# Optimization experiments

Hardware: AMD Instinct MI355X
Metric: run time of the kernel (lower is better)

Reference implementation:

```python
import jax, jax.numpy as jnp
import numpy as np

B, NV, NDIRS, NRINGS, NCH, NF = 2, 15000, 16, 3, 32, 64


def setup_inputs() -> dict:
    key = jax.random.key(0)
    k1, k2, k3, k4 = jax.random.split(key, 4)
    y = jax.random.normal(k1, (B, NV, NDIRS, NCH), dtype=jnp.float32)
    ft_v = jax.random.randint(k2, (NV, NRINGS, NDIRS), 0, NV, dtype=jnp.int32)
    ft_d = jax.random.randint(k3, (NV, NRINGS, NDIRS), 0, NDIRS, dtype=jnp.int32)
    kernel = jax.random.normal(k4, (NRINGS, NDIRS, NCH, NF), dtype=jnp.float32) * 0.05
    bias = jnp.zeros((NF,), dtype=jnp.float32)
    return {"y": y, "ft_v": ft_v, "ft_d": ft_d, "kernel": kernel, "bias": bias}


def reference(y, ft_v, ft_d, kernel, bias):
    # y: [b, nv, ndirs, nch]; ft_v/ft_d: [nv, nrings, ndirs]; kernel: [nrings, ndirs, nch, nf]
    b, nv, ndirs, nch = y.shape
    f = jnp.transpose(y, (1, 2, 3, 0))  # [nv, ndirs, nch, b]
    dirs = jnp.arange(ndirs)

    def per_dir(l):
        # cyclic forward shift of the direction axis, composed with the
        # frame-transporter gather: z[v,r,d,c,b] = f[ft_v[v,r,d], (ft_d[v,r,d]+l)%n, c, b]
        d_idx = (ft_d + l) % ndirs                # [nv, nrings, ndirs]
        z = f[ft_v, d_idx]                        # [nv, nrings, ndirs, nch, b]
        # kernel shifted in reverse: k_l[:, d] = kernel[:, (d-l)%n]
        k_l = kernel[:, (dirs - l) % ndirs]       # [nrings, ndirs, nch, nf]
        return jnp.einsum('vrdcb,rdcf->vbf', z, k_l)  # [nv, b, nf]

    out = jax.lax.map(per_dir, dirs)              # [ndirs, nv, b, nf] (sequential, like tf.while_loop)
    out = jnp.transpose(out, (2, 1, 0, 3))        # [b, nv, ndirs, nf]
    out = out + bias
    return jax.nn.relu(out)
```

## Files before the change

### kernel.cpp

```cpp
#include <hip/hip_runtime.h>

#define NV 15000
#define ND 16
#define NR 3
#define NC 32
#define NFDIM 64
#define BB 2

typedef short bf16x8 __attribute__((ext_vector_type(8)));
typedef float f32x4 __attribute__((ext_vector_type(4)));

#define YT_BYTES   30720000u
#define KB_OFF     30720000u
#define KB_BYTES   196608u
#define IDX_OFF    30916608u
#define IDX_BYTES  2880000u
#define WS_NEEDED  33796608u

__device__ __forceinline__ unsigned short f2bf(float x) {
  union { float f; unsigned int u; } cv; cv.f = x;
  unsigned int u = cv.u;
  u += 0x7FFF + ((u >> 16) & 1);
  return (unsigned short)(u >> 16);
}

__global__ void prep_y(const float* __restrict__ y, unsigned short* __restrict__ yt) {
  int tid = blockIdx.x * 256 + threadIdx.x;
  if (tid >= (NV * ND * BB * NC) / 8) return;
  int o   = tid * 8;
  int v   = o >> 10;
  int rem = o & 1023;
  int d   = rem >> 6;
  int b   = (rem >> 5) & 1;
  int c0  = rem & 31;
  const float* src = y + (((b * NV + v) * ND + d) * NC + c0);
  unsigned short* dst = yt + o;
#pragma unroll
  for (int i = 0; i < 8; i++) dst[i] = f2bf(src[i]);
}

__global__ void prep_kb(const float* __restrict__ kern, unsigned short* __restrict__ kb) {
  int t = blockIdx.x * 256 + threadIdx.x;
  if (t >= 48 * 4 * 64) return;
  int lane  = t & 63;
  int ft    = (t >> 6) & 3;
  int chunk = t >> 8;
  int q = lane >> 4;
  int f = ft * 16 + (lane & 15);
  unsigned short* dst = kb + t * 8;
#pragma unroll
  for (int j = 0; j < 8; j++) {
    int k = q * 8 + j;
    dst[j] = f2bf(kern[(chunk * NC + k) * NFDIM + f]);
  }
}

__global__ void prep_idx(const int* __restrict__ ftv, const int* __restrict__ ftd,
                         int* __restrict__ pidx) {
  int t = blockIdx.x * 256 + threadIdx.x;
  if (t >= NV * 48) return;
  pidx[t] = ftv[t] * 1024 + ftd[t] * 64;
}

__global__ __launch_bounds__(256, 4) void sync_conv_main(
    const unsigned short* __restrict__ yt, const unsigned short* __restrict__ kb,
    const int* __restrict__ pidx, const float* __restrict__ bias,
    float* __restrict__ out) {
  int tid  = threadIdx.x;
  int lane = tid & 63;
  int gid  = blockIdx.x * 4 + (tid >> 6);
  int l    = gid & 15;
  int mg   = gid >> 4;
  int q    = lane >> 4;
  int n    = lane & 15;
  int b    = n & 1;
  int voff = n >> 1;
  int vbase = mg * 32;

  int lane_elem = b * 32 + q * 8;
  const unsigned short* kb_lane = kb + lane * 8;

  f32x4 acc[4][4];
#pragma unroll
  for (int i = 0; i < 4; i++)
#pragma unroll
    for (int j = 0; j < 4; j++) acc[i][j] = (f32x4){0.f, 0.f, 0.f, 0.f};

  for (int r = 0; r < NR; r++) {
#pragma unroll 4
    for (int d = 0; d < ND; d++) {
      int dp = (d - l) & 15;
      const unsigned short* kbp = kb_lane + (r * 16 + dp) * 2048;
      bf16x8 bfr[4];
#pragma unroll
      for (int ft = 0; ft < 4; ft++)
        bfr[ft] = *reinterpret_cast<const bf16x8*>(kbp + ft * 512);
#pragma unroll
      for (int mt = 0; mt < 4; mt++) {
        int v = vbase + mt * 8 + voff;
        v = v < NV ? v : NV - 1;
        int p  = pidx[v * 48 + r * 16 + d];
        int dd = ((p >> 6) + l) & 15;
        int off = (p & 0xFFFFFC00) + (dd << 6) + lane_elem;
        bf16x8 afr = *reinterpret_cast<const bf16x8*>(yt + off);
#pragma unroll
        for (int ft = 0; ft < 4; ft++)
          acc[mt][ft] = __builtin_amdgcn_mfma_f32_16x16x32_bf16(
              afr, bfr[ft], acc[mt][ft], 0, 0, 0);
      }
    }
  }

  float bv[4];
#pragma unroll
  for (int ft = 0; ft < 4; ft++) bv[ft] = bias[ft * 16 + n];

#pragma unroll
  for (int mt = 0; mt < 4; mt++) {
#pragma unroll
    for (int reg = 0; reg < 4; reg++) {
      int m  = q * 4 + reg;
      int v  = vbase + mt * 8 + (m >> 1);
      int bb = m & 1;
      if (v < NV) {
        float* dst = out + (((bb * NV + v) * ND + l) * NFDIM) + n;
#pragma unroll
        for (int ft = 0; ft < 4; ft++) {
          float x = acc[mt][ft][reg] + bv[ft];
          dst[ft * 16] = x > 0.f ? x : 0.f;
        }
      }
    }
  }
}

__global__ void fallback_kernel(const float* __restrict__ y, const int* __restrict__ ftv,
                                const int* __restrict__ ftd, const float* __restrict__ kern,
                                const float* __restrict__ bias, float* __restrict__ out) {
  int idx = blockIdx.x;
  int l = idx & 15;
  int v = (idx >> 4) % NV;
  int b = idx / (NV * ND);
  int f = threadIdx.x;
  float acc = 0.f;
  for (int r = 0; r < NR; r++)
    for (int d = 0; d < ND; d++) {
      int ii = (v * NR + r) * ND + d;
      int vv = ftv[ii];
      int dd = (ftd[ii] + l) & 15;
      int dp = (d - l) & 15;
      const float* yp = y + ((b * NV + vv) * ND + dd) * NC;
      const float* kp = kern + ((r * 16 + dp) * NC) * NFDIM + f;
#pragma unroll 8
      for (int c = 0; c < NC; c++) acc += yp[c] * kp[c * NFDIM];
    }
  float x = acc + bias[f];
  out[idx * NFDIM + f] = x > 0.f ? x : 0.f;
}

extern "C" void kernel_launch(void* const* d_in, const int* in_sizes, int n_in,
                              void* d_out, int out_size, void* d_ws, size_t ws_size,
                              hipStream_t stream) {
  const float* y    = (const float*)d_in[0];
  const int*   ftv  = (const int*)d_in[1];
  const int*   ftd  = (const int*)d_in[2];
  const float* kern = (const float*)d_in[3];
  const float* bias = (const float*)d_in[4];
  float* out = (float*)d_out;

  if (ws_size >= (size_t)WS_NEEDED) {
    char* ws = (char*)d_ws;
    unsigned short* yt = (unsigned short*)ws;
    unsigned short* kb = (unsigned short*)(ws + KB_OFF);
    int* pidx          = (int*)(ws + IDX_OFF);

    prep_y<<<(NV * ND * BB * NC / 8 + 255) / 256, 256, 0, stream>>>(y, yt);
    prep_kb<<<(48 * 4 * 64 + 255) / 256, 256, 0, stream>>>(kern, kb);
    prep_idx<<<(NV * 48 + 255) / 256, 256, 0, stream>>>(ftv, ftd, pidx);
    sync_conv_main<<<1876, 256, 0, stream>>>(yt, kb, pidx, bias, out);
  } else {
    fallback_kernel<<<BB * NV * ND, NFDIM, 0, stream>>>(y, ftv, ftd, kern, bias, out);
  }
}
```

Measured before the change: 425.8 us.

## Stage gather indices in LDS, vectorize prep and output stores, reshape tiling

Drops the prep_idx kernel. Each block now loads its 16 vertices' ft_v/ft_d into shared memory, and its four waves cover four different shift values of l for the same vertices. The A-fragment gathers are batched four directions at a time ahead of the MFMAs so more loads are in flight. prep_y and the epilogue switch to vector loads and stores, and the output uses nontemporal float4 stores, enabled by permuting the kernel column layout so each lane owns four contiguous output features. The trade is more blocks with half the vertices per wave, plus an LDS staging pass and a barrier per block.

Measured after the change: 376.5 us. 11.6% less time.

```diff
diff --git a/kernel.cpp b/kernel.cpp
--- a/kernel.cpp
+++ b/kernel.cpp
@@ -9,13 +9,10 @@
 
 typedef short bf16x8 __attribute__((ext_vector_type(8)));
 typedef float f32x4 __attribute__((ext_vector_type(4)));
+typedef unsigned short u16x8 __attribute__((ext_vector_type(8)));
 
-#define YT_BYTES   30720000u
 #define KB_OFF     30720000u
-#define KB_BYTES   196608u
-#define IDX_OFF    30916608u
-#define IDX_BYTES  2880000u
-#define WS_NEEDED  33796608u
+#define WS_NEEDED  30916608u
 
 __device__ __forceinline__ unsigned short f2bf(float x) {
   union { float f; unsigned int u; } cv; cv.f = x;
@@ -24,7 +21,7 @@
   return (unsigned short)(u >> 16);
 }
 
-__global__ void prep_y(const float* __restrict__ y, unsigned short* __restrict__ yt) {
+__global__ void prep_y(const float* __restrict__ y, u16x8* __restrict__ yt) {
   int tid = blockIdx.x * 256 + threadIdx.x;
   if (tid >= (NV * ND * BB * NC) / 8) return;
   int o   = tid * 8;
@@ -33,10 +30,12 @@
   int d   = rem >> 6;
   int b   = (rem >> 5) & 1;
   int c0  = rem & 31;
-  const float* src = y + (((b * NV + v) * ND + d) * NC + c0);
-  unsigned short* dst = yt + o;
+  const f32x4* src = (const f32x4*)(y + (((b * NV + v) * ND + d) * NC + c0));
+  f32x4 lo = src[0], hi = src[1];
+  u16x8 r;
 #pragma unroll
-  for (int i = 0; i < 8; i++) dst[i] = f2bf(src[i]);
+  for (int i = 0; i < 4; i++) { r[i] = f2bf(lo[i]); r[4 + i] = f2bf(hi[i]); }
+  yt[tid] = r;
 }
 
 __global__ void prep_kb(const float* __restrict__ kern, unsigned short* __restrict__ kb) {
@@ -46,7 +45,7 @@
   int ft    = (t >> 6) & 3;
   int chunk = t >> 8;
   int q = lane >> 4;
-  int f = ft * 16 + (lane & 15);
+  int f = (lane & 15) * 4 + ft;
   unsigned short* dst = kb + t * 8;
 #pragma unroll
   for (int j = 0; j < 8; j++) {
@@ -55,80 +54,89 @@
   }
 }
 
-__global__ void prep_idx(const int* __restrict__ ftv, const int* __restrict__ ftd,
-                         int* __restrict__ pidx) {
-  int t = blockIdx.x * 256 + threadIdx.x;
-  if (t >= NV * 48) return;
-  pidx[t] = ftv[t] * 1024 + ftd[t] * 64;
-}
-
 __global__ __launch_bounds__(256, 4) void sync_conv_main(
     const unsigned short* __restrict__ yt, const unsigned short* __restrict__ kb,
-    const int* __restrict__ pidx, const float* __restrict__ bias,
-    float* __restrict__ out) {
+    const int* __restrict__ ftv, const int* __restrict__ ftd,
+    const float* __restrict__ bias, float* __restrict__ out) {
+  __shared__ int pidx_lds[16][49];
+
   int tid  = threadIdx.x;
   int lane = tid & 63;
-  int gid  = blockIdx.x * 4 + (tid >> 6);
-  int l    = gid & 15;
-  int mg   = gid >> 4;
+  int mg   = blockIdx.x >> 2;
+  int lg   = blockIdx.x & 3;
+  int l    = lg * 4 + (tid >> 6);
+  int vbase = mg * 16;
+
+  for (int t = tid; t < 16 * 48; t += 256) {
+    int i = t / 48, j = t - i * 48;
+    int v = vbase + i; v = v < NV ? v : NV - 1;
+    pidx_lds[i][j] = ftv[v * 48 + j] * 16 + (ftd[v * 48 + j] & 15);
+  }
+  __syncthreads();
+
   int q    = lane >> 4;
   int n    = lane & 15;
   int b    = n & 1;
   int voff = n >> 1;
-  int vbase = mg * 32;
-
   int lane_elem = b * 32 + q * 8;
   const unsigned short* kb_lane = kb + lane * 8;
 
-  f32x4 acc[4][4];
+  f32x4 acc[2][4];
 #pragma unroll
-  for (int i = 0; i < 4; i++)
+  for (int i = 0; i < 2; i++)
 #pragma unroll
     for (int j = 0; j < 4; j++) acc[i][j] = (f32x4){0.f, 0.f, 0.f, 0.f};
 
   for (int r = 0; r < NR; r++) {
-#pragma unroll 4
-    for (int d = 0; d < ND; d++) {
-      int dp = (d - l) & 15;
-      const unsigned short* kbp = kb_lane + (r * 16 + dp) * 2048;
-      bf16x8 bfr[4];
 #pragma unroll
-      for (int ft = 0; ft < 4; ft++)
-        bfr[ft] = *reinterpret_cast<const bf16x8*>(kbp + ft * 512);
+    for (int dg = 0; dg < 4; dg++) {
+      bf16x8 afr[2][4];
 #pragma unroll
-      for (int mt = 0; mt < 4; mt++) {
-        int v = vbase + mt * 8 + voff;
-        v = v < NV ? v : NV - 1;
-        int p  = pidx[v * 48 + r * 16 + d];
-        int dd = ((p >> 6) + l) & 15;
-        int off = (p & 0xFFFFFC00) + (dd << 6) + lane_elem;
-        bf16x8 afr = *reinterpret_cast<const bf16x8*>(yt + off);
+      for (int mt = 0; mt < 2; mt++)
+#pragma unroll
+        for (int ds = 0; ds < 4; ds++) {
+          int p  = pidx_lds[mt * 8 + voff][r * 16 + dg * 4 + ds];
+          int dd = ((p & 15) + l) & 15;
+          int off = (p >> 4) * 1024 + (dd << 6) + lane_elem;
+          afr[mt][ds] = *reinterpret_cast<const bf16x8*>(yt + off);
+        }
+#pragma unroll
+      for (int ds = 0; ds < 4; ds++) {
+        int d  = dg * 4 + ds;
+        int dp = (d - l) & 15;
+        const unsigned short* kbp = kb_lane + (r * 16 + dp) * 2048;
+        bf16x8 bfr[4];
 #pragma unroll
         for (int ft = 0; ft < 4; ft++)
-          acc[mt][ft] = __builtin_amdgcn_mfma_f32_16x16x32_bf16(
-              afr, bfr[ft], acc[mt][ft], 0, 0, 0);
+          bfr[ft] = *reinterpret_cast<const bf16x8*>(kbp + ft * 512);
+#pragma unroll
+        for (int mt = 0; mt < 2; mt++)
+#pragma unroll
+          for (int ft = 0; ft < 4; ft++)
+            acc[mt][ft] = __builtin_amdgcn_mfma_f32_16x16x32_bf16(
+                afr[mt][ds], bfr[ft], acc[mt][ft], 0, 0, 0);
       }
     }
   }
 
-  float bv[4];
-#pragma unroll
-  for (int ft = 0; ft < 4; ft++) bv[ft] = bias[ft * 16 + n];
+  f32x4 bv = *reinterpret_cast<const f32x4*>(bias + 4 * n);
 
 #pragma unroll
-  for (int mt = 0; mt < 4; mt++) {
+  for (int mt = 0; mt < 2; mt++) {
 #pragma unroll
     for (int reg = 0; reg < 4; reg++) {
       int m  = q * 4 + reg;
       int v  = vbase + mt * 8 + (m >> 1);
       int bb = m & 1;
       if (v < NV) {
-        float* dst = out + (((bb * NV + v) * ND + l) * NFDIM) + n;
+        f32x4 x;
 #pragma unroll
         for (int ft = 0; ft < 4; ft++) {
-          float x = acc[mt][ft][reg] + bv[ft];
-          dst[ft * 16] = x > 0.f ? x : 0.f;
+          float t = acc[mt][ft][reg] + bv[ft];
+          x[ft] = t > 0.f ? t : 0.f;
         }
+        float* dst = out + (((bb * NV + v) * ND + l) * NFDIM) + 4 * n;
+        __builtin_nontemporal_store(x, (f32x4*)dst);
       }
     }
   }
@@ -172,12 +180,10 @@
     char* ws = (char*)d_ws;
     unsigned short* yt = (unsigned short*)ws;
     unsigned short* kb = (unsigned short*)(ws + KB_OFF);
-    int* pidx          = (int*)(ws + IDX_OFF);
 
-    prep_y<<<(NV * ND * BB * NC / 8 + 255) / 256, 256, 0, stream>>>(y, yt);
+    prep_y<<<(NV * ND * BB * NC / 8 + 255) / 256, 256, 0, stream>>>(y, (u16x8*)yt);
     prep_kb<<<(48 * 4 * 64 + 255) / 256, 256, 0, stream>>>(kern, kb);
-    prep_idx<<<(NV * 48 + 255) / 256, 256, 0, stream>>>(ftv, ftd, pidx);
-    sync_conv_main<<<1876, 256, 0, stream>>>(yt, kb, pidx, bias, out);
+    sync_conv_main<<<3752, 256, 0, stream>>>(yt, kb, ftv, ftd, bias, out);
   } else {
     fallback_kernel<<<BB * NV * ND, NFDIM, 0, stream>>>(y, ftv, ftd, kern, bias, out);
   }
```
